# Optimization experiments

Hardware: AMD Instinct MI355X
Metric: run time of the kernel (lower is better)

The kernel has to match this reference:

```python
import jax, jax.numpy as jnp
import numpy as np

# Grid / physics constants (match init_kwargs)
NX, NY, NZ = 256, 256, 128
LX, LY, LZ = 1.0, 1.0, 1.0
CP, CV, MU, KTH, G = 1004.0, 717.0, 1.8e-5, 0.025, 9.8
DX = LX / NX            # periodic spacing in x
DY = LY / NY            # periodic spacing in y
DZ = LZ / (NZ - 1)      # non-periodic spacing in z


def _d1p(f, axis, d):
    # second-order central first derivative, periodic axis
    return (jnp.roll(f, -1, axis) - jnp.roll(f, 1, axis)) * (0.5 / d)


def _d2p(f, axis, d):
    # second-order central second derivative, periodic axis
    return (jnp.roll(f, -1, axis) + jnp.roll(f, 1, axis) - 2.0 * f) * (1.0 / (d * d))


def _d1z(f, d):
    # non-periodic first derivative along last axis: central interior, 2nd-order one-sided at walls
    inv2d = 0.5 / d
    c = (f[..., 2:] - f[..., :-2]) * inv2d
    lo = (-3.0 * f[..., 0:1] + 4.0 * f[..., 1:2] - f[..., 2:3]) * inv2d
    hi = (3.0 * f[..., -1:] - 4.0 * f[..., -2:-1] + f[..., -3:-2]) * inv2d
    return jnp.concatenate([lo, c, hi], axis=-1)


def _d2z(f, d):
    # non-periodic second derivative along last axis: central interior, 2nd-order one-sided at walls
    invd2 = 1.0 / (d * d)
    c = (f[..., 2:] - 2.0 * f[..., 1:-1] + f[..., :-2]) * invd2
    lo = (2.0 * f[..., 0:1] - 5.0 * f[..., 1:2] + 4.0 * f[..., 2:3] - f[..., 3:4]) * invd2
    hi = (2.0 * f[..., -1:] - 5.0 * f[..., -2:-1] + 4.0 * f[..., -3:-2] - f[..., -4:-3]) * invd2
    return jnp.concatenate([lo, c, hi], axis=-1)


def _lap(f):
    return _d2p(f, 0, DX) + _d2p(f, 1, DY) + _d2z(f, DZ)


def _adv(q, u, v, w):
    # u*dq/dx + v*dq/dy + w*dq/dz
    return u * _d1p(q, 0, DX) + v * _d1p(q, 1, DY) + w * _d1z(q, DZ)


def setup_inputs() -> dict:
    key = jax.random.key(0)
    state = 0.05 * jax.random.normal(key, (6, NX, NY, NZ), dtype=jnp.float32)
    # keep density positive and temperature physical (state order: u,v,w,rou,T,c)
    state = state.at[3].add(1.0)
    state = state.at[4].add(300.0)
    return {"state": state, "t": 0}


def reference(state, t):
    u, v, w, rou, T, c = state  # each [NX, NY, NZ]
    p = (CP - CV) * rou * T

    # NOTE: original code only applies -d/dx(rou*u) to drou; the y/z flux line is a no-op expression.
    drou = -_d1p(rou * u, 0, DX)

    du = (-_d1p(p, 0, DX) + MU * _lap(u)) / rou - _adv(u, u, v, w)
    dv = (-_d1p(p, 1, DY) + MU * _lap(v)) / rou - _adv(v, u, v, w)
    dw = (-G * rou - _d1z(p, DZ) + MU * _lap(w)) / rou - _adv(w, u, v, w)
    dT = KTH * _lap(T) / rou / CV - _adv(T, u, v, w)
    dc = -_adv(c, u, v, w)

    result = jnp.stack([du, dv, dw, drou, dT, dc], axis=0)
    # zero momentum and temperature tendencies at z walls
    result = result.at[0:3, :, :, 0].set(0.0)
    result = result.at[0:3, :, :, -1].set(0.0)
    result = result.at[4, :, :, 0].set(0.0)
    result = result.at[4, :, :, -1].set(0.0)
    return result
```

## Files before the change

kernel.cpp:

```cpp
#include <hip/hip_runtime.h>


namespace {
constexpr int NXc = 256, NYc = 256, NZc = 128;
constexpr int FS = NXc * NYc * NZc;
constexpr int XS = NYc * NZc;
constexpr int YS = NZc;

constexpr float CVc = 717.0f, MUc = 1.8e-5f, KTHc = 0.025f, Gc = 9.8f;
constexpr float Rgas = 1004.0f - 717.0f;

constexpr float inv2dx = 128.0f;
constexpr float inv2dy = 128.0f;
constexpr float inv2dz = 63.5f;
constexpr float invdx2 = 65536.0f;
constexpr float invdy2 = 65536.0f;
constexpr float invdz2 = 16129.0f;
}

__global__ __launch_bounds__(256) void rb_kernel(const float* __restrict__ s,
                                                 float* __restrict__ o) {
    const int z = threadIdx.x;
    const int y = blockIdx.x * 2 + threadIdx.y;
    const int x = blockIdx.y;

    const int xm = (x == 0) ? NXc - 1 : x - 1;
    const int xp = (x == NXc - 1) ? 0 : x + 1;
    const int ym = (y == 0) ? NYc - 1 : y - 1;
    const int yp = (y == NYc - 1) ? 0 : y + 1;

    const int b   = x * XS + y * YS + z;
    const int bxm = xm * XS + y * YS + z;
    const int bxp = xp * XS + y * YS + z;
    const int bym = x * XS + ym * YS + z;
    const int byp = x * XS + yp * YS + z;

    const float* su = s;
    const float* sv = s + FS;
    const float* sw = s + 2 * FS;
    const float* sr = s + 3 * FS;
    const float* st = s + 4 * FS;
    const float* sc = s + 5 * FS;

    const float u_c = su[b], v_c = sv[b], w_c = sw[b];
    const float r_c = sr[b], T_c = st[b], c_c = sc[b];

    const float u_xm = su[bxm], u_xp = su[bxp];
    const float r_xm = sr[bxm], r_xp = sr[bxp];
    const float c_xm = sc[bxm], c_xp = sc[bxp];
    const float c_ym = sc[bym], c_yp = sc[byp];

    const float drou = -(r_xp * u_xp - r_xm * u_xm) * inv2dx;

    float dzc;
    if (z == 0) {
        dzc = (-3.0f * c_c + 4.0f * sc[b + 1] - sc[b + 2]) * inv2dz;
    } else if (z == NZc - 1) {
        dzc = (3.0f * c_c - 4.0f * sc[b - 1] + sc[b - 2]) * inv2dz;
    } else {
        dzc = (sc[b + 1] - sc[b - 1]) * inv2dz;
    }
    const float dc = -(u_c * (c_xp - c_xm) * inv2dx +
                       v_c * (c_yp - c_ym) * inv2dy +
                       w_c * dzc);

    float du = 0.0f, dv = 0.0f, dw = 0.0f, dT = 0.0f;

    if (z > 0 && z < NZc - 1) {
        const float u_ym = su[bym], u_yp = su[byp];
        const float u_zm = su[b - 1], u_zp = su[b + 1];
        const float v_xm = sv[bxm], v_xp = sv[bxp];
        const float v_ym = sv[bym], v_yp = sv[byp];
        const float v_zm = sv[b - 1], v_zp = sv[b + 1];
        const float w_xm = sw[bxm], w_xp = sw[bxp];
        const float w_ym = sw[bym], w_yp = sw[byp];
        const float w_zm = sw[b - 1], w_zp = sw[b + 1];
        const float T_xm = st[bxm], T_xp = st[bxp];
        const float T_ym = st[bym], T_yp = st[byp];
        const float T_zm = st[b - 1], T_zp = st[b + 1];
        const float r_ym = sr[bym], r_yp = sr[byp];
        const float r_zm = sr[b - 1], r_zp = sr[b + 1];

        const float inv_r = 1.0f / r_c;

        const float p_xm = Rgas * r_xm * T_xm, p_xp = Rgas * r_xp * T_xp;
        const float p_ym = Rgas * r_ym * T_ym, p_yp = Rgas * r_yp * T_yp;
        const float p_zm = Rgas * r_zm * T_zm, p_zp = Rgas * r_zp * T_zp;

        const float dpdx = (p_xp - p_xm) * inv2dx;
        const float dpdy = (p_yp - p_ym) * inv2dy;
        const float dpdz = (p_zp - p_zm) * inv2dz;

        const float lap_u = (u_xp + u_xm - 2.0f * u_c) * invdx2 +
                            (u_yp + u_ym - 2.0f * u_c) * invdy2 +
                            (u_zp + u_zm - 2.0f * u_c) * invdz2;
        const float lap_v = (v_xp + v_xm - 2.0f * v_c) * invdx2 +
                            (v_yp + v_ym - 2.0f * v_c) * invdy2 +
                            (v_zp + v_zm - 2.0f * v_c) * invdz2;
        const float lap_w = (w_xp + w_xm - 2.0f * w_c) * invdx2 +
                            (w_yp + w_ym - 2.0f * w_c) * invdy2 +
                            (w_zp + w_zm - 2.0f * w_c) * invdz2;
        const float lap_T = (T_xp + T_xm - 2.0f * T_c) * invdx2 +
                            (T_yp + T_ym - 2.0f * T_c) * invdy2 +
                            (T_zp + T_zm - 2.0f * T_c) * invdz2;

        const float adv_u = u_c * (u_xp - u_xm) * inv2dx +
                            v_c * (u_yp - u_ym) * inv2dy +
                            w_c * (u_zp - u_zm) * inv2dz;
        const float adv_v = u_c * (v_xp - v_xm) * inv2dx +
                            v_c * (v_yp - v_ym) * inv2dy +
                            w_c * (v_zp - v_zm) * inv2dz;
        const float adv_w = u_c * (w_xp - w_xm) * inv2dx +
                            v_c * (w_yp - w_ym) * inv2dy +
                            w_c * (w_zp - w_zm) * inv2dz;
        const float adv_T = u_c * (T_xp - T_xm) * inv2dx +
                            v_c * (T_yp - T_ym) * inv2dy +
                            w_c * (T_zp - T_zm) * inv2dz;

        du = (-dpdx + MUc * lap_u) * inv_r - adv_u;
        dv = (-dpdy + MUc * lap_v) * inv_r - adv_v;
        dw = (-Gc * r_c - dpdz + MUc * lap_w) * inv_r - adv_w;
        dT = (KTHc * lap_T) * inv_r * (1.0f / CVc) - adv_T;
    }

    o[b]          = du;
    o[b + FS]     = dv;
    o[b + 2 * FS] = dw;
    o[b + 3 * FS] = drou;
    o[b + 4 * FS] = dT;
    o[b + 5 * FS] = dc;
}

extern "C" void kernel_launch(void* const* d_in, const int* in_sizes, int n_in,
                              void* d_out, int out_size, void* d_ws, size_t ws_size,
                              hipStream_t stream) {
    (void)in_sizes; (void)n_in; (void)d_ws; (void)ws_size; (void)out_size;
    const float* s = (const float*)d_in[0];
    float* o = (float*)d_out;

    dim3 block(128, 2, 1);
    dim3 grid(NYc / 2, NXc, 1);
    rb_kernel<<<grid, block, 0, stream>>>(s, o);
}
```

Before: 373.9 us.

## Vectorize stencil to float4 per thread with warp shuffles for z-neighbors

Each thread now handles four consecutive z points through float4 loads and stores. A 32-lane group covers one z column of 128 points, and the z-neighbours come from __shfl_up/__shfl_down instead of extra global loads. The per-point branching on interior versus wall is replaced by fix-ups on lanes 0 and 31. This cuts the number of memory instructions and the redundant z-neighbour reads, in exchange for higher register pressure per thread and a dependence on warp-width-32 shuffle semantics within a wave64 wavefront.

After: 350.1 us. 1.07x faster.

```diff
diff --git a/kernel.cpp b/kernel.cpp
--- a/kernel.cpp
+++ b/kernel.cpp
@@ -7,21 +7,43 @@
 constexpr int XS = NYc * NZc;
 constexpr int YS = NZc;
 
-constexpr float CVc = 717.0f, MUc = 1.8e-5f, KTHc = 0.025f, Gc = 9.8f;
-constexpr float Rgas = 1004.0f - 717.0f;
+constexpr float MUc = 1.8e-5f, KTHc = 0.025f, Gc = 9.8f;
+constexpr float Rgas = 287.0f;
+constexpr float invCV = 1.0f / 717.0f;
 
-constexpr float inv2dx = 128.0f;
-constexpr float inv2dy = 128.0f;
-constexpr float inv2dz = 63.5f;
-constexpr float invdx2 = 65536.0f;
-constexpr float invdy2 = 65536.0f;
-constexpr float invdz2 = 16129.0f;
+constexpr float inv2dx = 128.0f, inv2dy = 128.0f, inv2dz = 63.5f;
+constexpr float invdx2 = 65536.0f, invdy2 = 65536.0f, invdz2 = 16129.0f;
 }
+
+__device__ __forceinline__ float4 ld4(const float* __restrict__ p, int i4) {
+    return reinterpret_cast<const float4*>(p)[i4];
+}
+
+#define LOADN(q, sq) \
+    const float4 q##_xm = ld4(sq, bxm4), q##_xp = ld4(sq, bxp4); \
+    const float4 q##_ym = ld4(sq, bym4), q##_yp = ld4(sq, byp4); \
+    const float q##_zm = __shfl_up(q##_c.w, 1, 32); \
+    const float q##_zp = __shfl_down(q##_c.x, 1, 32);
+
+#define ADV_LAP_C(q, C, PREV, NEXT) \
+    adv_##q.C = u_c.C * (q##_xp.C - q##_xm.C) * inv2dx \
+              + v_c.C * (q##_yp.C - q##_ym.C) * inv2dy \
+              + w_c.C * ((NEXT) - (PREV)) * inv2dz; \
+    lap_##q.C = (q##_xp.C + q##_xm.C - 2.0f * q##_c.C) * invdx2 \
+              + (q##_yp.C + q##_ym.C - 2.0f * q##_c.C) * invdy2 \
+              + ((NEXT) + (PREV) - 2.0f * q##_c.C) * invdz2;
+
+#define DERIVS(q) \
+    float4 adv_##q, lap_##q; \
+    ADV_LAP_C(q, x, q##_zm,  q##_c.y) \
+    ADV_LAP_C(q, y, q##_c.x, q##_c.z) \
+    ADV_LAP_C(q, z, q##_c.y, q##_c.w) \
+    ADV_LAP_C(q, w, q##_c.z, q##_zp)
 
 __global__ __launch_bounds__(256) void rb_kernel(const float* __restrict__ s,
                                                  float* __restrict__ o) {
-    const int z = threadIdx.x;
-    const int y = blockIdx.x * 2 + threadIdx.y;
+    const int l = threadIdx.x;
+    const int y = blockIdx.x * 8 + threadIdx.y;
     const int x = blockIdx.y;
 
     const int xm = (x == 0) ? NXc - 1 : x - 1;
@@ -29,11 +51,11 @@
     const int ym = (y == 0) ? NYc - 1 : y - 1;
     const int yp = (y == NYc - 1) ? 0 : y + 1;
 
-    const int b   = x * XS + y * YS + z;
-    const int bxm = xm * XS + y * YS + z;
-    const int bxp = xp * XS + y * YS + z;
-    const int bym = x * XS + ym * YS + z;
-    const int byp = x * XS + yp * YS + z;
+    const int b4   = (x * XS + y * YS) / 4 + l;
+    const int bxm4 = (xm * XS + y * YS) / 4 + l;
+    const int bxp4 = (xp * XS + y * YS) / 4 + l;
+    const int bym4 = (x * XS + ym * YS) / 4 + l;
+    const int byp4 = (x * XS + yp * YS) / 4 + l;
 
     const float* su = s;
     const float* sv = s + FS;
@@ -42,93 +64,88 @@
     const float* st = s + 4 * FS;
     const float* sc = s + 5 * FS;
 
-    const float u_c = su[b], v_c = sv[b], w_c = sw[b];
-    const float r_c = sr[b], T_c = st[b], c_c = sc[b];
+    const float4 u_c = ld4(su, b4), v_c = ld4(sv, b4), w_c = ld4(sw, b4);
+    const float4 r_c = ld4(sr, b4), T_c = ld4(st, b4), c_c = ld4(sc, b4);
 
-    const float u_xm = su[bxm], u_xp = su[bxp];
-    const float r_xm = sr[bxm], r_xp = sr[bxp];
-    const float c_xm = sc[bxm], c_xp = sc[bxp];
-    const float c_ym = sc[bym], c_yp = sc[byp];
+    float4 inv_r;
+    inv_r.x = 1.0f / r_c.x; inv_r.y = 1.0f / r_c.y;
+    inv_r.z = 1.0f / r_c.z; inv_r.w = 1.0f / r_c.w;
 
-    const float drou = -(r_xp * u_xp - r_xm * u_xm) * inv2dx;
+    LOADN(T, st)
+    DERIVS(T)
+    LOADN(r, sr)
 
-    float dzc;
-    if (z == 0) {
-        dzc = (-3.0f * c_c + 4.0f * sc[b + 1] - sc[b + 2]) * inv2dz;
-    } else if (z == NZc - 1) {
-        dzc = (3.0f * c_c - 4.0f * sc[b - 1] + sc[b - 2]) * inv2dz;
-    } else {
-        dzc = (sc[b + 1] - sc[b - 1]) * inv2dz;
+    float4 p_c, p_xm, p_xp, p_ym, p_yp;
+#define PC(C) \
+    p_c.C  = Rgas * r_c.C  * T_c.C; \
+    p_xm.C = Rgas * r_xm.C * T_xm.C;  p_xp.C = Rgas * r_xp.C * T_xp.C; \
+    p_ym.C = Rgas * r_ym.C * T_ym.C;  p_yp.C = Rgas * r_yp.C * T_yp.C;
+    PC(x) PC(y) PC(z) PC(w)
+#undef PC
+    const float p_zm = __shfl_up(p_c.w, 1, 32);
+    const float p_zp = __shfl_down(p_c.x, 1, 32);
+
+    float4 dpdx, dpdy, dpdz;
+#define DP(C) \
+    dpdx.C = (p_xp.C - p_xm.C) * inv2dx; \
+    dpdy.C = (p_yp.C - p_ym.C) * inv2dy;
+    DP(x) DP(y) DP(z) DP(w)
+#undef DP
+    dpdz.x = (p_c.y - p_zm) * inv2dz;
+    dpdz.y = (p_c.z - p_c.x) * inv2dz;
+    dpdz.z = (p_c.w - p_c.y) * inv2dz;
+    dpdz.w = (p_zp  - p_c.z) * inv2dz;
+
+    LOADN(u, su)
+    DERIVS(u)
+    float4 drou;
+#define DR(C) drou.C = -(r_xp.C * u_xp.C - r_xm.C * u_xm.C) * inv2dx;
+    DR(x) DR(y) DR(z) DR(w)
+#undef DR
+
+    LOADN(v, sv)
+    DERIVS(v)
+
+    LOADN(w, sw)
+    DERIVS(w)
+
+    LOADN(c, sc)
+    DERIVS(c)
+    (void)lap_c;
+
+    float4 du4, dv4, dw4, dT4, dc4;
+#define OUT(C) \
+    du4.C = (-dpdx.C + MUc * lap_u.C) * inv_r.C - adv_u.C; \
+    dv4.C = (-dpdy.C + MUc * lap_v.C) * inv_r.C - adv_v.C; \
+    dw4.C = (-Gc * r_c.C - dpdz.C + MUc * lap_w.C) * inv_r.C - adv_w.C; \
+    dT4.C = KTHc * lap_T.C * inv_r.C * invCV - adv_T.C; \
+    dc4.C = -adv_c.C;
+    OUT(x) OUT(y) OUT(z) OUT(w)
+#undef OUT
+
+    if (l == 0) {
+        du4.x = 0.0f; dv4.x = 0.0f; dw4.x = 0.0f; dT4.x = 0.0f;
+        const float dzc0 = (-3.0f * c_c.x + 4.0f * c_c.y - c_c.z) * inv2dz;
+        dc4.x = -(u_c.x * (c_xp.x - c_xm.x) * inv2dx
+                + v_c.x * (c_yp.x - c_ym.x) * inv2dy
+                + w_c.x * dzc0);
     }
-    const float dc = -(u_c * (c_xp - c_xm) * inv2dx +
-                       v_c * (c_yp - c_ym) * inv2dy +
-                       w_c * dzc);
-
-    float du = 0.0f, dv = 0.0f, dw = 0.0f, dT = 0.0f;
-
-    if (z > 0 && z < NZc - 1) {
-        const float u_ym = su[bym], u_yp = su[byp];
-        const float u_zm = su[b - 1], u_zp = su[b + 1];
-        const float v_xm = sv[bxm], v_xp = sv[bxp];
-        const float v_ym = sv[bym], v_yp = sv[byp];
-        const float v_zm = sv[b - 1], v_zp = sv[b + 1];
-        const float w_xm = sw[bxm], w_xp = sw[bxp];
-        const float w_ym = sw[bym], w_yp = sw[byp];
-        const float w_zm = sw[b - 1], w_zp = sw[b + 1];
-        const float T_xm = st[bxm], T_xp = st[bxp];
-        const float T_ym = st[bym], T_yp = st[byp];
-        const float T_zm = st[b - 1], T_zp = st[b + 1];
-        const float r_ym = sr[bym], r_yp = sr[byp];
-        const float r_zm = sr[b - 1], r_zp = sr[b + 1];
-
-        const float inv_r = 1.0f / r_c;
-
-        const float p_xm = Rgas * r_xm * T_xm, p_xp = Rgas * r_xp * T_xp;
-        const float p_ym = Rgas * r_ym * T_ym, p_yp = Rgas * r_yp * T_yp;
-        const float p_zm = Rgas * r_zm * T_zm, p_zp = Rgas * r_zp * T_zp;
-
-        const float dpdx = (p_xp - p_xm) * inv2dx;
-        const float dpdy = (p_yp - p_ym) * inv2dy;
-        const float dpdz = (p_zp - p_zm) * inv2dz;
-
-        const float lap_u = (u_xp + u_xm - 2.0f * u_c) * invdx2 +
-                            (u_yp + u_ym - 2.0f * u_c) * invdy2 +
-                            (u_zp + u_zm - 2.0f * u_c) * invdz2;
-        const float lap_v = (v_xp + v_xm - 2.0f * v_c) * invdx2 +
-                            (v_yp + v_ym - 2.0f * v_c) * invdy2 +
-                            (v_zp + v_zm - 2.0f * v_c) * invdz2;
-        const float lap_w = (w_xp + w_xm - 2.0f * w_c) * invdx2 +
-                            (w_yp + w_ym - 2.0f * w_c) * invdy2 +
-                            (w_zp + w_zm - 2.0f * w_c) * invdz2;
-        const float lap_T = (T_xp + T_xm - 2.0f * T_c) * invdx2 +
-                            (T_yp + T_ym - 2.0f * T_c) * invdy2 +
-                            (T_zp + T_zm - 2.0f * T_c) * invdz2;
-
-        const float adv_u = u_c * (u_xp - u_xm) * inv2dx +
-                            v_c * (u_yp - u_ym) * inv2dy +
-                            w_c * (u_zp - u_zm) * inv2dz;
-        const float adv_v = u_c * (v_xp - v_xm) * inv2dx +
-                            v_c * (v_yp - v_ym) * inv2dy +
-                            w_c * (v_zp - v_zm) * inv2dz;
-        const float adv_w = u_c * (w_xp - w_xm) * inv2dx +
-                            v_c * (w_yp - w_ym) * inv2dy +
-                            w_c * (w_zp - w_zm) * inv2dz;
-        const float adv_T = u_c * (T_xp - T_xm) * inv2dx +
-                            v_c * (T_yp - T_ym) * inv2dy +
-                            w_c * (T_zp - T_zm) * inv2dz;
-
-        du = (-dpdx + MUc * lap_u) * inv_r - adv_u;
-        dv = (-dpdy + MUc * lap_v) * inv_r - adv_v;
-        dw = (-Gc * r_c - dpdz + MUc * lap_w) * inv_r - adv_w;
-        dT = (KTHc * lap_T) * inv_r * (1.0f / CVc) - adv_T;
+    if (l == 31) {
+        du4.w = 0.0f; dv4.w = 0.0f; dw4.w = 0.0f; dT4.w = 0.0f;
+        const float dzcN = (3.0f * c_c.w - 4.0f * c_c.z + c_c.y) * inv2dz;
+        dc4.w = -(u_c.w * (c_xp.w - c_xm.w) * inv2dx
+                + v_c.w * (c_yp.w - c_ym.w) * inv2dy
+                + w_c.w * dzcN);
     }
 
-    o[b]          = du;
-    o[b + FS]     = dv;
-    o[b + 2 * FS] = dw;
-    o[b + 3 * FS] = drou;
-    o[b + 4 * FS] = dT;
-    o[b + 5 * FS] = dc;
+    float4* o4 = reinterpret_cast<float4*>(o);
+    const int fs4 = FS / 4;
+    o4[b4]           = du4;
+    o4[b4 + fs4]     = dv4;
+    o4[b4 + 2 * fs4] = dw4;
+    o4[b4 + 3 * fs4] = drou;
+    o4[b4 + 4 * fs4] = dT4;
+    o4[b4 + 5 * fs4] = dc4;
 }
 
 extern "C" void kernel_launch(void* const* d_in, const int* in_sizes, int n_in,
@@ -138,7 +155,7 @@
     const float* s = (const float*)d_in[0];
     float* o = (float*)d_out;
 
-    dim3 block(128, 2, 1);
-    dim3 grid(NYc / 2, NXc, 1);
+    dim3 block(32, 8, 1);
+    dim3 grid(NYc / 8, NXc, 1);
     rb_kernel<<<grid, block, 0, stream>>>(s, o);
 }
```
